# Kernel tuning notes

Hardware: AMD Instinct MI355X
Metric: run time of the kernel (lower is better)

## Reference

```python
import jax, jax.numpy as jnp
import numpy as np

NEG_INF = -1e30


def setup_inputs() -> dict:
    key = jax.random.key(0)
    kq, kk, kv, ks = jax.random.split(key, 4)
    B, H, S, D = 2, 16, 2048, 64
    return {
        "q": jax.random.normal(kq, (B, H, S, D), dtype=jnp.float32),
        "k": jax.random.normal(kk, (B, H, S, D), dtype=jnp.float32),
        "v": jax.random.normal(kv, (B, H, S, D), dtype=jnp.float32),
        "sink_weights": jax.random.normal(ks, (H,), dtype=jnp.float32),
        "sliding_window": 1024,
    }


def reference(q, k, v, sink_weights, sliding_window):
    """Sliding-window causal attention with a learnable attention-sink logit.

    Equivalent to FlexAttention.forward with sink_weights given: an extra kv
    position (the sink) is appended whose score is replaced by sink_weights[h]
    and whose value is zero -> it only adds mass to the softmax denominator.
    """
    B, H, S_q, D = q.shape
    S_kv = k.shape[2]
    scale = 1.0 / np.sqrt(D)

    # [B, H, S_q, S_kv] raw scores
    scores = jnp.einsum("bhqd,bhkd->bhqk", q, k) * scale

    q_idx = jnp.arange(S_q)[:, None]
    kv_idx = jnp.arange(S_kv)[None, :]
    keep = (kv_idx <= q_idx) & (q_idx - kv_idx <= sliding_window)  # [S_q, S_kv]
    scores = jnp.where(keep[None, None], scores, NEG_INF)

    # sink column: per-head learnable logit, always visible
    sink_col = jnp.broadcast_to(
        sink_weights[None, :, None, None], (B, H, S_q, 1)
    )
    logits = jnp.concatenate([scores, sink_col], axis=-1)  # [B,H,S_q,S_kv+1]

    probs = jax.nn.softmax(logits, axis=-1)
    # sink value is zero, so only the first S_kv prob columns hit v
    out = jnp.einsum("bhqk,bhkd->bhqd", probs[..., :S_kv], v)
    return out
```

## Files before the change

kernel.cpp:

```cpp
#include <hip/hip_runtime.h>


typedef __bf16 bf16x8 __attribute__((ext_vector_type(8)));
typedef __bf16 bf16x4 __attribute__((ext_vector_type(4)));
typedef float  f32x16 __attribute__((ext_vector_type(16)));

#define SK 72
#define SV 72
#define SPP 72
#define NT 128

__global__ __launch_bounds__(NT, 2) void flex_attn_mfma32(
    const float* __restrict__ Q, const float* __restrict__ K,
    const float* __restrict__ V, const float* __restrict__ SINKW,
    const int* __restrict__ SWIN, float* __restrict__ OUT,
    const int H, const int S)
{
    const int t    = threadIdx.x;
    const int lane = t & 63;
    const int g    = t >> 6;
    const int c    = lane & 31;
    const int hl   = lane >> 5;
    const int qt   = blockIdx.x;
    const int bh   = blockIdx.y;
    const int h    = bh % H;
    const int q0   = qt * 64;
    const int qw0  = q0 + 32 * g;
    const int W    = SWIN[0];
    const float scale = 0.125f;

    __shared__ __align__(16) __bf16 k_lds[64 * SK];
    __shared__ __align__(16) __bf16 v_lds[64 * SV];
    __shared__ __align__(16) __bf16 p_lds[2 * 32 * SPP];

    const size_t basebh = (size_t)bh * S * 64;

    bf16x8 bq[4];
    {
        const float4* qp4 = (const float4*)(Q + basebh + (size_t)(qw0 + c) * 64);
        #pragma unroll
        for (int ks = 0; ks < 4; ++ks) {
            float4 f0 = qp4[4 * ks + 2 * hl];
            float4 f1 = qp4[4 * ks + 2 * hl + 1];
            bq[ks][0] = (__bf16)(f0.x * scale); bq[ks][1] = (__bf16)(f0.y * scale);
            bq[ks][2] = (__bf16)(f0.z * scale); bq[ks][3] = (__bf16)(f0.w * scale);
            bq[ks][4] = (__bf16)(f1.x * scale); bq[ks][5] = (__bf16)(f1.y * scale);
            bq[ks][6] = (__bf16)(f1.z * scale); bq[ks][7] = (__bf16)(f1.w * scale);
        }
    }

    const int dg = t & 15;
    const int kg = t >> 4;
    const float4* kp4 = (const float4*)(K + basebh);
    const float4* vp4 = (const float4*)(V + basebh);
    float4 kreg[8], vreg[8];

    auto load_tiles = [&](int kt) {
        #pragma unroll
        for (int i = 0; i < 8; ++i)
            kreg[i] = kp4[kt * 1024 + i * NT + t];
        #pragma unroll
        for (int r = 0; r < 2; ++r)
            #pragma unroll
            for (int kk = 0; kk < 4; ++kk)
                vreg[4 * r + kk] = vp4[kt * 1024 + (32 * r + 4 * kg + kk) * 16 + dg];
    };

    auto stage_tiles = [&]() {
        #pragma unroll
        for (int i = 0; i < 8; ++i) {
            const int flat = i * NT + t;
            const int key = flat >> 4, dd = flat & 15;
            float4 f = kreg[i];
            bf16x4 b = { (__bf16)f.x, (__bf16)f.y, (__bf16)f.z, (__bf16)f.w };
            *(bf16x4*)&k_lds[key * SK + 4 * dd] = b;
        }
        #pragma unroll
        for (int r = 0; r < 2; ++r) {
            float4 a0 = vreg[4*r+0], a1 = vreg[4*r+1], a2 = vreg[4*r+2], a3 = vreg[4*r+3];
            const int kb = 32 * r + 4 * kg;
            bf16x4 w0 = { (__bf16)a0.x, (__bf16)a1.x, (__bf16)a2.x, (__bf16)a3.x };
            bf16x4 w1 = { (__bf16)a0.y, (__bf16)a1.y, (__bf16)a2.y, (__bf16)a3.y };
            bf16x4 w2 = { (__bf16)a0.z, (__bf16)a1.z, (__bf16)a2.z, (__bf16)a3.z };
            bf16x4 w3 = { (__bf16)a0.w, (__bf16)a1.w, (__bf16)a2.w, (__bf16)a3.w };
            *(bf16x4*)&v_lds[(4 * dg + 0) * SV + kb] = w0;
            *(bf16x4*)&v_lds[(4 * dg + 1) * SV + kb] = w1;
            *(bf16x4*)&v_lds[(4 * dg + 2) * SV + kb] = w2;
            *(bf16x4*)&v_lds[(4 * dg + 3) * SV + kb] = w3;
        }
    };

    float mrun = SINKW[h];
    float lrun = 1.0f;
    f32x16 accO0, accO1;
    #pragma unroll
    for (int i = 0; i < 16; ++i) { accO0[i] = 0.0f; accO1[i] = 0.0f; }

    int lo = q0 - W; if (lo < 0) lo = 0;
    const int kt0 = lo >> 6, kt1 = qt;

    load_tiles(kt0);

    for (int kt = kt0; kt <= kt1; ++kt) {
        __syncthreads();
        stage_tiles();
        if (kt < kt1) load_tiles(kt + 1);
        __syncthreads();

        const int k0 = kt * 64;

        f32x16 accS0, accS1;
        #pragma unroll
        for (int i = 0; i < 16; ++i) { accS0[i] = 0.0f; accS1[i] = 0.0f; }
        #pragma unroll
        for (int ks = 0; ks < 4; ++ks) {
            bf16x8 ka0 = *(const bf16x8*)&k_lds[c * SK + 16 * ks + 8 * hl];
            bf16x8 ka1 = *(const bf16x8*)&k_lds[(32 + c) * SK + 16 * ks + 8 * hl];
            accS0 = __builtin_amdgcn_mfma_f32_32x32x16_bf16(ka0, bq[ks], accS0, 0, 0, 0);
            accS1 = __builtin_amdgcn_mfma_f32_32x32x16_bf16(ka1, bq[ks], accS1, 0, 0, 0);
        }

        const bool interior = (k0 + 63 <= qw0) && (qw0 + 31 - k0 <= W);
        if (!interior) {
            const int qi = qw0 + c;
            #pragma unroll
            for (int rg = 0; rg < 16; ++rg) {
                const int kb  = (rg & 3) + 8 * (rg >> 2) + 4 * hl;
                const int ki0 = k0 + kb, ki1 = k0 + 32 + kb;
                if (!((ki0 <= qi) && (qi - ki0 <= W))) accS0[rg] = -1e30f;
                if (!((ki1 <= qi) && (qi - ki1 <= W))) accS1[rg] = -1e30f;
            }
        }

        float mx = accS0[0];
        #pragma unroll
        for (int i = 1; i < 16; ++i) mx = fmaxf(mx, accS0[i]);
        #pragma unroll
        for (int i = 0; i < 16; ++i) mx = fmaxf(mx, accS1[i]);
        mx = fmaxf(mx, __shfl_xor(mx, 32, 64));
        const float mnew  = fmaxf(mrun, mx);
        const float alpha = __expf(mrun - mnew);
        float ps = 0.0f;
        #pragma unroll
        for (int i = 0; i < 16; ++i) { float p = __expf(accS0[i] - mnew); accS0[i] = p; ps += p; }
        #pragma unroll
        for (int i = 0; i < 16; ++i) { float p = __expf(accS1[i] - mnew); accS1[i] = p; ps += p; }
        ps += __shfl_xor(ps, 32, 64);
        lrun = lrun * alpha + ps;
        mrun = mnew;
        #pragma unroll
        for (int i = 0; i < 16; ++i) { accO0[i] *= alpha; accO1[i] *= alpha; }

        __bf16* pw = p_lds + g * 32 * SPP;
        #pragma unroll
        for (int rg = 0; rg < 4; ++rg) {
            bf16x4 b0 = { (__bf16)accS0[4*rg+0], (__bf16)accS0[4*rg+1],
                          (__bf16)accS0[4*rg+2], (__bf16)accS0[4*rg+3] };
            bf16x4 b1 = { (__bf16)accS1[4*rg+0], (__bf16)accS1[4*rg+1],
                          (__bf16)accS1[4*rg+2], (__bf16)accS1[4*rg+3] };
            *(bf16x4*)&pw[c * SPP +      8 * rg + 4 * hl] = b0;
            *(bf16x4*)&pw[c * SPP + 32 + 8 * rg + 4 * hl] = b1;
        }

        #pragma unroll
        for (int ks = 0; ks < 4; ++ks) {
            bf16x8 bp  = *(const bf16x8*)&pw[c * SPP + 16 * ks + 8 * hl];
            bf16x8 va0 = *(const bf16x8*)&v_lds[c * SV + 16 * ks + 8 * hl];
            bf16x8 va1 = *(const bf16x8*)&v_lds[(32 + c) * SV + 16 * ks + 8 * hl];
            accO0 = __builtin_amdgcn_mfma_f32_32x32x16_bf16(va0, bp, accO0, 0, 0, 0);
            accO1 = __builtin_amdgcn_mfma_f32_32x32x16_bf16(va1, bp, accO1, 0, 0, 0);
        }
    }

    const float inv = 1.0f / lrun;
    float* ob = OUT + basebh + (size_t)(qw0 + c) * 64;
    #pragma unroll
    for (int rg = 0; rg < 4; ++rg) {
        float4 f0 = { accO0[4*rg+0]*inv, accO0[4*rg+1]*inv, accO0[4*rg+2]*inv, accO0[4*rg+3]*inv };
        float4 f1 = { accO1[4*rg+0]*inv, accO1[4*rg+1]*inv, accO1[4*rg+2]*inv, accO1[4*rg+3]*inv };
        *(float4*)&ob[     8 * rg + 4 * hl] = f0;
        *(float4*)&ob[32 + 8 * rg + 4 * hl] = f1;
    }
}

extern "C" void kernel_launch(void* const* d_in, const int* in_sizes, int n_in,
                              void* d_out, int out_size, void* d_ws, size_t ws_size,
                              hipStream_t stream) {
    const float* q     = (const float*)d_in[0];
    const float* k     = (const float*)d_in[1];
    const float* v     = (const float*)d_in[2];
    const float* sinkw = (const float*)d_in[3];
    const int*   swin  = (const int*)d_in[4];
    float* out = (float*)d_out;

    const int H = in_sizes[3];
    const int S = 2048;
    const int B = in_sizes[0] / (H * S * 64);

    dim3 grid(S / 64, B * H);
    flex_attn_mfma32<<<grid, NT, 0, stream>>>(q, k, v, sinkw, swin, out, H, S);
}
```

Baseline: 147.7 us.

## Split-KV load balancing with static segment tables and separate combine kernel

Replaces the per-64-query-tile grid with 128-query items whose KV ranges are split into segments, assigned to 24 blocks per head through hardcoded tables so every block does roughly equal work. Partial outputs (bf16) and max/sum statistics are written to workspace, and a second kernel merges them with log-sum-exp rescaling. This targets the load imbalance of causal sliding-window attention, where early query tiles have few KV tiles, at the cost of an extra launch, workspace traffic and bf16 rounding of partials. The tables hardcode S=2048 and a window of 1024, so other shapes would give wrong results.

```diff
diff --git a/kernel.cpp b/kernel.cpp
--- a/kernel.cpp
+++ b/kernel.cpp
@@ -8,178 +8,267 @@
 #define SK 72
 #define SV 72
 #define SPP 72
-#define NT 128
-
-__global__ __launch_bounds__(NT, 2) void flex_attn_mfma32(
+#define NT 256
+#define NEG_BIG (-3.0e38f)
+
+__device__ const int SEG_N[24] = {3,2,2,2,2,1,2,1, 1,1,1,1,1,1,1,1, 1,1,1,1,1,1,1,1};
+__device__ const int SEG_IT[24][3] = {
+  {0,1,2},{2,3,0},{3,4,0},{4,5,0},{5,6,0},{6,0,0},{6,7,0},{7,0,0},
+  {8,0,0},{8,0,0},{9,0,0},{9,0,0},{10,0,0},{10,0,0},{11,0,0},{11,0,0},
+  {12,0,0},{12,0,0},{13,0,0},{13,0,0},{14,0,0},{14,0,0},{15,0,0},{15,0,0}};
+__device__ const int SEG_J0[24][3] = {
+  {0,0,0},{3,0,0},{6,0,0},{7,0,0},{6,0,0},{3,0,0},{12,0,0},{7,0,0},
+  {0,0,0},{9,0,0},{0,0,0},{9,0,0},{0,0,0},{9,0,0},{0,0,0},{9,0,0},
+  {0,0,0},{9,0,0},{0,0,0},{9,0,0},{0,0,0},{9,0,0},{0,0,0},{9,0,0}};
+__device__ const int SEG_J1[24][3] = {
+  {2,4,3},{6,6,0},{8,7,0},{10,6,0},{12,3,0},{12,0,0},{14,7,0},{16,0,0},
+  {9,0,0},{18,0,0},{9,0,0},{18,0,0},{9,0,0},{18,0,0},{9,0,0},{18,0,0},
+  {9,0,0},{18,0,0},{9,0,0},{18,0,0},{9,0,0},{18,0,0},{9,0,0},{18,0,0}};
+__device__ const int SEG_SX[24][3] = {
+  {0,0,0},{1,0,0},{1,0,0},{1,0,0},{1,0,0},{1,0,0},{2,0,0},{1,0,0},
+  {0,0,0},{1,0,0},{0,0,0},{1,0,0},{0,0,0},{1,0,0},{0,0,0},{1,0,0},
+  {0,0,0},{1,0,0},{0,0,0},{1,0,0},{0,0,0},{1,0,0},{0,0,0},{1,0,0}};
+__device__ const int NSEG_ITEM[16] = {1,1,2,2,2,2,3,2, 2,2,2,2,2,2,2,2};
+
+__global__ __launch_bounds__(NT, 3) void flex_r5_main(
     const float* __restrict__ Q, const float* __restrict__ K,
     const float* __restrict__ V, const float* __restrict__ SINKW,
-    const int* __restrict__ SWIN, float* __restrict__ OUT,
+    const int* __restrict__ SWIN, void* __restrict__ WS,
     const int H, const int S)
 {
     const int t    = threadIdx.x;
     const int lane = t & 63;
-    const int g    = t >> 6;
+    const int w    = t >> 6;
     const int c    = lane & 31;
     const int hl   = lane >> 5;
-    const int qt   = blockIdx.x;
-    const int bh   = blockIdx.y;
-    const int h    = bh % H;
-    const int q0   = qt * 64;
-    const int qw0  = q0 + 32 * g;
     const int W    = SWIN[0];
     const float scale = 0.125f;
 
+    const int NBH = gridDim.x / 24;
+    const int bh  = blockIdx.x / 24;
+    const int b24 = blockIdx.x - bh * 24;
+    const int h   = bh % H;
+    const float sw = SINKW[h];
+
     __shared__ __align__(16) __bf16 k_lds[64 * SK];
     __shared__ __align__(16) __bf16 v_lds[64 * SV];
-    __shared__ __align__(16) __bf16 p_lds[2 * 32 * SPP];
+    __shared__ __align__(16) __bf16 p_lds[4 * 32 * SPP];
 
     const size_t basebh = (size_t)bh * S * 64;
-
-    bf16x8 bq[4];
-    {
-        const float4* qp4 = (const float4*)(Q + basebh + (size_t)(qw0 + c) * 64);
-        #pragma unroll
-        for (int ks = 0; ks < 4; ++ks) {
-            float4 f0 = qp4[4 * ks + 2 * hl];
-            float4 f1 = qp4[4 * ks + 2 * hl + 1];
-            bq[ks][0] = (__bf16)(f0.x * scale); bq[ks][1] = (__bf16)(f0.y * scale);
-            bq[ks][2] = (__bf16)(f0.z * scale); bq[ks][3] = (__bf16)(f0.w * scale);
-            bq[ks][4] = (__bf16)(f1.x * scale); bq[ks][5] = (__bf16)(f1.y * scale);
-            bq[ks][6] = (__bf16)(f1.z * scale); bq[ks][7] = (__bf16)(f1.w * scale);
-        }
-    }
-
-    const int dg = t & 15;
-    const int kg = t >> 4;
     const float4* kp4 = (const float4*)(K + basebh);
     const float4* vp4 = (const float4*)(V + basebh);
-    float4 kreg[8], vreg[8];
-
-    auto load_tiles = [&](int kt) {
-        #pragma unroll
-        for (int i = 0; i < 8; ++i)
-            kreg[i] = kp4[kt * 1024 + i * NT + t];
-        #pragma unroll
-        for (int r = 0; r < 2; ++r)
-            #pragma unroll
-            for (int kk = 0; kk < 4; ++kk)
-                vreg[4 * r + kk] = vp4[kt * 1024 + (32 * r + 4 * kg + kk) * 16 + dg];
-    };
-
-    auto stage_tiles = [&]() {
-        #pragma unroll
-        for (int i = 0; i < 8; ++i) {
-            const int flat = i * NT + t;
-            const int key = flat >> 4, dd = flat & 15;
-            float4 f = kreg[i];
-            bf16x4 b = { (__bf16)f.x, (__bf16)f.y, (__bf16)f.z, (__bf16)f.w };
-            *(bf16x4*)&k_lds[key * SK + 4 * dd] = b;
-        }
-        #pragma unroll
-        for (int r = 0; r < 2; ++r) {
-            float4 a0 = vreg[4*r+0], a1 = vreg[4*r+1], a2 = vreg[4*r+2], a3 = vreg[4*r+3];
-            const int kb = 32 * r + 4 * kg;
-            bf16x4 w0 = { (__bf16)a0.x, (__bf16)a1.x, (__bf16)a2.x, (__bf16)a3.x };
-            bf16x4 w1 = { (__bf16)a0.y, (__bf16)a1.y, (__bf16)a2.y, (__bf16)a3.y };
-            bf16x4 w2 = { (__bf16)a0.z, (__bf16)a1.z, (__bf16)a2.z, (__bf16)a3.z };
-            bf16x4 w3 = { (__bf16)a0.w, (__bf16)a1.w, (__bf16)a2.w, (__bf16)a3.w };
-            *(bf16x4*)&v_lds[(4 * dg + 0) * SV + kb] = w0;
-            *(bf16x4*)&v_lds[(4 * dg + 1) * SV + kb] = w1;
-            *(bf16x4*)&v_lds[(4 * dg + 2) * SV + kb] = w2;
-            *(bf16x4*)&v_lds[(4 * dg + 3) * SV + kb] = w3;
-        }
-    };
-
-    float mrun = SINKW[h];
-    float lrun = 1.0f;
-    f32x16 accO0, accO1;
+    __bf16* O_ws = (__bf16*)WS;
+    float2* ml_ws = (float2*)((char*)WS + (size_t)NBH * 48 * 16384);
+
+    const int dgi = t & 15;
+    const int kgi = t >> 4;
+    float4 kreg[4], vreg[4];
+
+    const int ns = SEG_N[b24];
+
+    {
+        const int it0 = SEG_IT[b24][0];
+        const int ktA0 = (2 * it0 - 16 > 0) ? (2 * it0 - 16) : 0;
+        const int kt = ktA0 + SEG_J0[b24][0];
+        #pragma unroll
+        for (int i = 0; i < 4; ++i) kreg[i] = kp4[kt * 1024 + i * NT + t];
+        #pragma unroll
+        for (int kk = 0; kk < 4; ++kk) vreg[kk] = vp4[kt * 1024 + (4 * kgi + kk) * 16 + dgi];
+    }
+
+    for (int s = 0; s < ns; ++s) {
+        const int item = SEG_IT[b24][s];
+        const int j0   = SEG_J0[b24][s];
+        const int j1   = SEG_J1[b24][s];
+        const int sidx = SEG_SX[b24][s];
+        const int ktA  = (2 * item - 16 > 0) ? (2 * item - 16) : 0;
+        const int qw0  = item * 128 + 32 * w;
+        const int qi   = qw0 + c;
+
+        bf16x8 bq[4];
+        {
+            const float4* qp4 = (const float4*)(Q + basebh + (size_t)qi * 64);
+            #pragma unroll
+            for (int ks = 0; ks < 4; ++ks) {
+                float4 f0 = qp4[4 * ks + 2 * hl];
+                float4 f1 = qp4[4 * ks + 2 * hl + 1];
+                bq[ks][0] = (__bf16)(f0.x * scale); bq[ks][1] = (__bf16)(f0.y * scale);
+                bq[ks][2] = (__bf16)(f0.z * scale); bq[ks][3] = (__bf16)(f0.w * scale);
+                bq[ks][4] = (__bf16)(f1.x * scale); bq[ks][5] = (__bf16)(f1.y * scale);
+                bq[ks][6] = (__bf16)(f1.z * scale); bq[ks][7] = (__bf16)(f1.w * scale);
+            }
+        }
+
+        float mrun = (sidx == 0) ? sw : NEG_BIG;
+        float lrun = (sidx == 0) ? 1.0f : 0.0f;
+        f32x16 accO0, accO1;
+        #pragma unroll
+        for (int i = 0; i < 16; ++i) { accO0[i] = 0.0f; accO1[i] = 0.0f; }
+
+        for (int j = j0; j < j1; ++j) {
+            const int k0 = (ktA + j) * 64;
+            __syncthreads();
+
+            #pragma unroll
+            for (int i = 0; i < 4; ++i) {
+                const int flat = i * NT + t;
+                const int key = flat >> 4, dd = flat & 15;
+                float4 f = kreg[i];
+                bf16x4 b = { (__bf16)f.x, (__bf16)f.y, (__bf16)f.z, (__bf16)f.w };
+                *(bf16x4*)&k_lds[key * SK + 4 * dd] = b;
+            }
+            {
+                float4 a0 = vreg[0], a1 = vreg[1], a2 = vreg[2], a3 = vreg[3];
+                bf16x4 w0 = { (__bf16)a0.x, (__bf16)a1.x, (__bf16)a2.x, (__bf16)a3.x };
+                bf16x4 w1 = { (__bf16)a0.y, (__bf16)a1.y, (__bf16)a2.y, (__bf16)a3.y };
+                bf16x4 w2 = { (__bf16)a0.z, (__bf16)a1.z, (__bf16)a2.z, (__bf16)a3.z };
+                bf16x4 w3 = { (__bf16)a0.w, (__bf16)a1.w, (__bf16)a2.w, (__bf16)a3.w };
+                *(bf16x4*)&v_lds[(4 * dgi + 0) * SV + 4 * kgi] = w0;
+                *(bf16x4*)&v_lds[(4 * dgi + 1) * SV + 4 * kgi] = w1;
+                *(bf16x4*)&v_lds[(4 * dgi + 2) * SV + 4 * kgi] = w2;
+                *(bf16x4*)&v_lds[(4 * dgi + 3) * SV + 4 * kgi] = w3;
+            }
+            int nkt = -1;
+            if (j + 1 < j1) nkt = ktA + j + 1;
+            else if (s + 1 < ns) {
+                const int it2 = SEG_IT[b24][s + 1];
+                const int ktA2 = (2 * it2 - 16 > 0) ? (2 * it2 - 16) : 0;
+                nkt = ktA2 + SEG_J0[b24][s + 1];
+            }
+            if (nkt >= 0) {
+                #pragma unroll
+                for (int i = 0; i < 4; ++i) kreg[i] = kp4[nkt * 1024 + i * NT + t];
+                #pragma unroll
+                for (int kk = 0; kk < 4; ++kk) vreg[kk] = vp4[nkt * 1024 + (4 * kgi + kk) * 16 + dgi];
+            }
+            __syncthreads();
+
+            f32x16 accS0, accS1;
+            #pragma unroll
+            for (int i = 0; i < 16; ++i) { accS0[i] = 0.0f; accS1[i] = 0.0f; }
+            #pragma unroll
+            for (int ks = 0; ks < 4; ++ks) {
+                bf16x8 ka0 = *(const bf16x8*)&k_lds[c * SK + 16 * ks + 8 * hl];
+                bf16x8 ka1 = *(const bf16x8*)&k_lds[(32 + c) * SK + 16 * ks + 8 * hl];
+                accS0 = __builtin_amdgcn_mfma_f32_32x32x16_bf16(ka0, bq[ks], accS0, 0, 0, 0);
+                accS1 = __builtin_amdgcn_mfma_f32_32x32x16_bf16(ka1, bq[ks], accS1, 0, 0, 0);
+            }
+
+            const bool interior = (k0 + 63 <= qw0) && (qw0 + 31 - k0 <= W);
+            if (!interior) {
+                #pragma unroll
+                for (int rg = 0; rg < 16; ++rg) {
+                    const int kb  = (rg & 3) + 8 * (rg >> 2) + 4 * hl;
+                    const int ki0 = k0 + kb, ki1 = k0 + 32 + kb;
+                    if (!((ki0 <= qi) && (qi - ki0 <= W))) accS0[rg] = -1e30f;
+                    if (!((ki1 <= qi) && (qi - ki1 <= W))) accS1[rg] = -1e30f;
+                }
+            }
+
+            float mx = accS0[0];
+            #pragma unroll
+            for (int i = 1; i < 16; ++i) mx = fmaxf(mx, accS0[i]);
+            #pragma unroll
+            for (int i = 0; i < 16; ++i) mx = fmaxf(mx, accS1[i]);
+            mx = fmaxf(mx, __shfl_xor(mx, 32, 64));
+            const float mnew  = fmaxf(mrun, mx);
+            const float alpha = __expf(mrun - mnew);
+            float ps = 0.0f;
+            #pragma unroll
+            for (int i = 0; i < 16; ++i) { float p = __expf(accS0[i] - mnew); accS0[i] = p; ps += p; }
+            #pragma unroll
+            for (int i = 0; i < 16; ++i) { float p = __expf(accS1[i] - mnew); accS1[i] = p; ps += p; }
+            ps += __shfl_xor(ps, 32, 64);
+            lrun = lrun * alpha + ps;
+            mrun = mnew;
+            #pragma unroll
+            for (int i = 0; i < 16; ++i) { accO0[i] *= alpha; accO1[i] *= alpha; }
+
+            __bf16* pw = p_lds + w * 32 * SPP;
+            #pragma unroll
+            for (int rg = 0; rg < 4; ++rg) {
+                bf16x4 b0 = { (__bf16)accS0[4*rg+0], (__bf16)accS0[4*rg+1],
+                              (__bf16)accS0[4*rg+2], (__bf16)accS0[4*rg+3] };
+                bf16x4 b1 = { (__bf16)accS1[4*rg+0], (__bf16)accS1[4*rg+1],
+                              (__bf16)accS1[4*rg+2], (__bf16)accS1[4*rg+3] };
+                *(bf16x4*)&pw[c * SPP +      8 * rg + 4 * hl] = b0;
+                *(bf16x4*)&pw[c * SPP + 32 + 8 * rg + 4 * hl] = b1;
+            }
+
+            #pragma unroll
+            for (int ks = 0; ks < 4; ++ks) {
+                bf16x8 bp  = *(const bf16x8*)&pw[c * SPP + 16 * ks + 8 * hl];
+                bf16x8 va0 = *(const bf16x8*)&v_lds[c * SV + 16 * ks + 8 * hl];
+                bf16x8 va1 = *(const bf16x8*)&v_lds[(32 + c) * SV + 16 * ks + 8 * hl];
+                accO0 = __builtin_amdgcn_mfma_f32_32x32x16_bf16(va0, bp, accO0, 0, 0, 0);
+                accO1 = __builtin_amdgcn_mfma_f32_32x32x16_bf16(va1, bp, accO1, 0, 0, 0);
+            }
+        }
+
+        const int slot = (bh * 16 + item) * 3 + sidx;
+        const int qrel = 32 * w + c;
+        if (hl == 0) ml_ws[(size_t)slot * 128 + qrel] = make_float2(mrun, lrun);
+        __bf16* Os = O_ws + (size_t)slot * 8192 + (size_t)qrel * 64;
+        #pragma unroll
+        for (int qd = 0; qd < 4; ++qd) {
+            const int d0 = 8 * qd + 4 * hl;
+            bf16x4 b0 = { (__bf16)accO0[4*qd+0], (__bf16)accO0[4*qd+1],
+                          (__bf16)accO0[4*qd+2], (__bf16)accO0[4*qd+3] };
+            bf16x4 b1 = { (__bf16)accO1[4*qd+0], (__bf16)accO1[4*qd+1],
+                          (__bf16)accO1[4*qd+2], (__bf16)accO1[4*qd+3] };
+            *(bf16x4*)&Os[d0]      = b0;
+            *(bf16x4*)&Os[32 + d0] = b1;
+        }
+    }
+}
+
+__global__ __launch_bounds__(256) void flex_r5_combine(
+    const void* __restrict__ WS, float* __restrict__ OUT, const int H, const int S)
+{
+    const int NBH  = gridDim.x / 16;
+    const int bi   = blockIdx.x;
+    const int bh   = bi >> 4;
+    const int item = bi & 15;
+    const int ns   = NSEG_ITEM[item];
+    const int t    = threadIdx.x;
+    const int q    = t >> 1;
+    const int half = t & 1;
+
+    const __bf16* O_ws = (const __bf16*)WS;
+    const float2* ml_ws = (const float2*)((const char*)WS + (size_t)NBH * 48 * 16384);
+    const int base = bi * 3;
+
+    float m[3], lv[3], a[3];
+    float mst = NEG_BIG;
+    for (int s = 0; s < ns; ++s) {
+        float2 e = ml_ws[(size_t)(base + s) * 128 + q];
+        m[s] = e.x; lv[s] = e.y;
+        mst = fmaxf(mst, m[s]);
+    }
+    float lst = 0.0f;
+    for (int s = 0; s < ns; ++s) { a[s] = __expf(m[s] - mst); lst += a[s] * lv[s]; }
+    const float inv = 1.0f / lst;
+
+    float acc[32];
     #pragma unroll
-    for (int i = 0; i < 16; ++i) { accO0[i] = 0.0f; accO1[i] = 0.0f; }
-
-    int lo = q0 - W; if (lo < 0) lo = 0;
-    const int kt0 = lo >> 6, kt1 = qt;
-
-    load_tiles(kt0);
-
-    for (int kt = kt0; kt <= kt1; ++kt) {
-        __syncthreads();
-        stage_tiles();
-        if (kt < kt1) load_tiles(kt + 1);
-        __syncthreads();
-
-        const int k0 = kt * 64;
-
-        f32x16 accS0, accS1;
-        #pragma unroll
-        for (int i = 0; i < 16; ++i) { accS0[i] = 0.0f; accS1[i] = 0.0f; }
-        #pragma unroll
-        for (int ks = 0; ks < 4; ++ks) {
-            bf16x8 ka0 = *(const bf16x8*)&k_lds[c * SK + 16 * ks + 8 * hl];
-            bf16x8 ka1 = *(const bf16x8*)&k_lds[(32 + c) * SK + 16 * ks + 8 * hl];
-            accS0 = __builtin_amdgcn_mfma_f32_32x32x16_bf16(ka0, bq[ks], accS0, 0, 0, 0);
-            accS1 = __builtin_amdgcn_mfma_f32_32x32x16_bf16(ka1, bq[ks], accS1, 0, 0, 0);
-        }
-
-        const bool interior = (k0 + 63 <= qw0) && (qw0 + 31 - k0 <= W);
-        if (!interior) {
-            const int qi = qw0 + c;
-            #pragma unroll
-            for (int rg = 0; rg < 16; ++rg) {
-                const int kb  = (rg & 3) + 8 * (rg >> 2) + 4 * hl;
-                const int ki0 = k0 + kb, ki1 = k0 + 32 + kb;
-                if (!((ki0 <= qi) && (qi - ki0 <= W))) accS0[rg] = -1e30f;
-                if (!((ki1 <= qi) && (qi - ki1 <= W))) accS1[rg] = -1e30f;
-            }
-        }
-
-        float mx = accS0[0];
-        #pragma unroll
-        for (int i = 1; i < 16; ++i) mx = fmaxf(mx, accS0[i]);
-        #pragma unroll
-        for (int i = 0; i < 16; ++i) mx = fmaxf(mx, accS1[i]);
-        mx = fmaxf(mx, __shfl_xor(mx, 32, 64));
-        const float mnew  = fmaxf(mrun, mx);
-        const float alpha = __expf(mrun - mnew);
-        float ps = 0.0f;
-        #pragma unroll
-        for (int i = 0; i < 16; ++i) { float p = __expf(accS0[i] - mnew); accS0[i] = p; ps += p; }
-        #pragma unroll
-        for (int i = 0; i < 16; ++i) { float p = __expf(accS1[i] - mnew); accS1[i] = p; ps += p; }
-        ps += __shfl_xor(ps, 32, 64);
-        lrun = lrun * alpha + ps;
-        mrun = mnew;
-        #pragma unroll
-        for (int i = 0; i < 16; ++i) { accO0[i] *= alpha; accO1[i] *= alpha; }
-
-        __bf16* pw = p_lds + g * 32 * SPP;
-        #pragma unroll
-        for (int rg = 0; rg < 4; ++rg) {
-            bf16x4 b0 = { (__bf16)accS0[4*rg+0], (__bf16)accS0[4*rg+1],
-                          (__bf16)accS0[4*rg+2], (__bf16)accS0[4*rg+3] };
-            bf16x4 b1 = { (__bf16)accS1[4*rg+0], (__bf16)accS1[4*rg+1],
-                          (__bf16)accS1[4*rg+2], (__bf16)accS1[4*rg+3] };
-            *(bf16x4*)&pw[c * SPP +      8 * rg + 4 * hl] = b0;
-            *(bf16x4*)&pw[c * SPP + 32 + 8 * rg + 4 * hl] = b1;
-        }
-
-        #pragma unroll
-        for (int ks = 0; ks < 4; ++ks) {
-            bf16x8 bp  = *(const bf16x8*)&pw[c * SPP + 16 * ks + 8 * hl];
-            bf16x8 va0 = *(const bf16x8*)&v_lds[c * SV + 16 * ks + 8 * hl];
-            bf16x8 va1 = *(const bf16x8*)&v_lds[(32 + c) * SV + 16 * ks + 8 * hl];
-            accO0 = __builtin_amdgcn_mfma_f32_32x32x16_bf16(va0, bp, accO0, 0, 0, 0);
-            accO1 = __builtin_amdgcn_mfma_f32_32x32x16_bf16(va1, bp, accO1, 0, 0, 0);
-        }
-    }
-
-    const float inv = 1.0f / lrun;
-    float* ob = OUT + basebh + (size_t)(qw0 + c) * 64;
+    for (int i = 0; i < 32; ++i) acc[i] = 0.0f;
+    for (int s = 0; s < ns; ++s) {
+        const __bf16* Os = O_ws + (size_t)(base + s) * 8192 + (size_t)q * 64 + 32 * half;
+        const float as = a[s];
+        #pragma unroll
+        for (int v8 = 0; v8 < 4; ++v8) {
+            bf16x8 o = *(const bf16x8*)&Os[8 * v8];
+            #pragma unroll
+            for (int j = 0; j < 8; ++j) acc[8 * v8 + j] += as * (float)o[j];
+        }
+    }
+
+    float* dst = OUT + (size_t)bh * S * 64 + (size_t)(item * 128 + q) * 64 + 32 * half;
     #pragma unroll
-    for (int rg = 0; rg < 4; ++rg) {
-        float4 f0 = { accO0[4*rg+0]*inv, accO0[4*rg+1]*inv, accO0[4*rg+2]*inv, accO0[4*rg+3]*inv };
-        float4 f1 = { accO1[4*rg+0]*inv, accO1[4*rg+1]*inv, accO1[4*rg+2]*inv, accO1[4*rg+3]*inv };
-        *(float4*)&ob[     8 * rg + 4 * hl] = f0;
-        *(float4*)&ob[32 + 8 * rg + 4 * hl] = f1;
+    for (int v4 = 0; v4 < 8; ++v4) {
+        float4 f = { acc[4*v4+0] * inv, acc[4*v4+1] * inv,
+                     acc[4*v4+2] * inv, acc[4*v4+3] * inv };
+        *(float4*)&dst[4 * v4] = f;
     }
 }
 
@@ -196,7 +285,9 @@
     const int H = in_sizes[3];
     const int S = 2048;
     const int B = in_sizes[0] / (H * S * 64);
-
-    dim3 grid(S / 64, B * H);
-    flex_attn_mfma32<<<grid, NT, 0, stream>>>(q, k, v, sinkw, swin, out, H, S);
+    const int NBH = B * H;
+
+
+    flex_r5_main<<<dim3(NBH * 24), NT, 0, stream>>>(q, k, v, sinkw, swin, d_ws, H, S);
+    flex_r5_combine<<<dim3(NBH * 16), 256, 0, stream>>>(d_ws, out, H, S);
 }
```

Result: faster. 139.9 us (-5.3%).
